# Kernel optimization log

Measured on AMD Instinct MI355X. Metric: run time of the kernel, lower is better.

## Reference

```python
import jax, jax.numpy as jnp
import numpy as np

D_MODEL = 1024
N_HEAD = 16
D_HEAD = D_MODEL // N_HEAD
SEQ = 1024
RLEN = 2 * SEQ
BATCH = 4
LN_EPS = 1e-5


def setup_inputs() -> dict:
    key = jax.random.key(0)
    ks = jax.random.split(key, 12)
    s = 0.02
    return {
        "h": jax.random.normal(ks[0], (SEQ, BATCH, D_MODEL), jnp.float32),
        "r": jax.random.normal(ks[1], (RLEN, BATCH, D_MODEL), jnp.float32),
        "q_w": jax.random.normal(ks[2], (D_MODEL, N_HEAD, D_HEAD), jnp.float32) * s,
        "k_w": jax.random.normal(ks[3], (D_MODEL, N_HEAD, D_HEAD), jnp.float32) * s,
        "v_w": jax.random.normal(ks[4], (D_MODEL, N_HEAD, D_HEAD), jnp.float32) * s,
        "o_w": jax.random.normal(ks[5], (D_MODEL, N_HEAD, D_HEAD), jnp.float32) * s,
        "r_w": jax.random.normal(ks[6], (D_MODEL, N_HEAD, D_HEAD), jnp.float32) * s,
        "r_r_bias": jax.random.normal(ks[7], (N_HEAD, D_HEAD), jnp.float32) * s,
        "r_w_bias": jax.random.normal(ks[8], (N_HEAD, D_HEAD), jnp.float32) * s,
        "ln_gamma": jnp.ones((D_MODEL,), jnp.float32),
        "ln_beta": jnp.zeros((D_MODEL,), jnp.float32),
    }


def rel_shift_bnij(x, klen):
    # x: [b, n, i, j]; Transformer-XL relative-shift trick
    b, n, i, j = x.shape
    x = x.reshape(b, n, j, i)[:, :, 1:, :].reshape(b, n, i, j - 1)
    return x[:, :, :, :klen]


def reference(h, r, q_w, k_w, v_w, o_w, r_w, r_r_bias, r_w_bias, ln_gamma, ln_beta):
    scale = 1.0 / np.sqrt(D_HEAD).astype(np.float32)
    # projections: i=seq, b=batch, n=heads, d=head dim
    q_head = jnp.einsum('ibh,hnd->ibnd', h, q_w)
    k_head = jnp.einsum('ibh,hnd->ibnd', h, k_w)
    v_head = jnp.einsum('ibh,hnd->ibnd', h, v_w)
    k_head_r = jnp.einsum('ibh,hnd->ibnd', r, r_w)
    # content and position attention scores
    ac = jnp.einsum('ibnd,jbnd->bnij', q_head + r_w_bias, k_head)
    bd = jnp.einsum('ibnd,jbnd->bnij', q_head + r_r_bias, k_head_r)
    bd = rel_shift_bnij(bd, klen=ac.shape[3])
    attn_prob = jax.nn.softmax((ac + bd) * scale, axis=3)  # dropout is identity at eval
    attn_vec = jnp.einsum('bnij,jbnd->ibnd', attn_prob, v_head)
    attn_out = jnp.einsum('ibnd,hnd->ibh', attn_vec, o_w) + h  # residual
    mu = jnp.mean(attn_out, axis=-1, keepdims=True)
    var = jnp.var(attn_out, axis=-1, keepdims=True)
    return (attn_out - mu) / jnp.sqrt(var + LN_EPS) * ln_gamma + ln_beta
```

## Files before the change

### kernel.cpp

```cpp
#include <hip/hip_runtime.h>
#include <stdint.h>


typedef __attribute__((ext_vector_type(8))) short v8s;
typedef __attribute__((ext_vector_type(4))) float v4f;

__device__ __forceinline__ uint16_t f2b(float x) {
    uint32_t u = __builtin_bit_cast(uint32_t, x);
    u += 0x7fffu + ((u >> 16) & 1u);
    return (uint16_t)(u >> 16);
}

__device__ __forceinline__ void gld16(const void* g, void* lds) {
    __builtin_amdgcn_global_load_lds(
        (const __attribute__((address_space(1))) uint32_t*)g,
        (__attribute__((address_space(3))) uint32_t*)lds, 16, 0, 0);
}

__global__ __launch_bounds__(256) void convert_cast(
    const float4* __restrict__ h4, const float4* __restrict__ r4,
    const float4* __restrict__ w4,
    uint64_t* __restrict__ hB, uint64_t* __restrict__ rB, uint64_t* __restrict__ owB)
{
    const int total = 1048576 + 2097152 + 262144;
    for (int i = blockIdx.x * 256 + threadIdx.x; i < total; i += gridDim.x * 256) {
        float4 v; uint64_t* dst; int idx;
        if (i < 1048576)      { idx = i;           v = h4[idx]; dst = hB; }
        else if (i < 3145728) { idx = i - 1048576; v = r4[idx]; dst = rB; }
        else                  { idx = i - 3145728; v = w4[idx]; dst = owB; }
        uint64_t p = (uint64_t)f2b(v.x) | ((uint64_t)f2b(v.y) << 16)
                   | ((uint64_t)f2b(v.z) << 32) | ((uint64_t)f2b(v.w) << 48);
        dst[idx] = p;
    }
}

__global__ __launch_bounds__(256) void transpose_w(
    const float* __restrict__ q_w, const float* __restrict__ k_w,
    const float* __restrict__ v_w, const float* __restrict__ r_w,
    uint16_t* __restrict__ Wcat, uint16_t* __restrict__ rwT)
{
    __shared__ float t[64][65];
    const int n0 = blockIdx.x * 64, h0 = blockIdx.y * 64, z = blockIdx.z;
    const float* src = (z == 0) ? q_w : (z == 1) ? k_w : (z == 2) ? v_w : r_w;
    uint16_t* dst = (z == 3) ? rwT : Wcat + (size_t)z * 1048576;
    const int tid = threadIdx.x;
#pragma unroll
    for (int q = 0; q < 16; ++q) {
        int idx = q * 256 + tid, rr = idx >> 6, cc = idx & 63;
        t[rr][cc] = src[(size_t)(h0 + rr) * 1024 + n0 + cc];
    }
    __syncthreads();
#pragma unroll
    for (int q = 0; q < 16; ++q) {
        int idx = q * 256 + tid, rr = idx >> 6, cc = idx & 63;
        dst[(size_t)(n0 + rr) * 1024 + h0 + cc] = f2b(t[cc][rr]);
    }
}

template<int MODE>
__global__ __launch_bounds__(256) void gemm_bt(
    const uint16_t* __restrict__ A, const uint16_t* __restrict__ B, int K,
    uint16_t* __restrict__ o0, uint16_t* __restrict__ o1,
    uint16_t* __restrict__ o2, uint16_t* __restrict__ o3,
    const float* __restrict__ bias0, const float* __restrict__ bias1,
    float* __restrict__ fo, const float* __restrict__ fres)
{
    __shared__ __align__(16) uint16_t As[128 * 64];
    __shared__ __align__(16) uint16_t Bs[128 * 64];
    const int tid = threadIdx.x;
    const int w = tid >> 6, lane = tid & 63;
    const int g = lane >> 4, c15 = lane & 15;
    const int m0 = blockIdx.y * 128, n0 = blockIdx.x * 128;
    const int wr = w >> 1, wc = w & 1;

    int rowq[4], colq[4];
#pragma unroll
    for (int q = 0; q < 4; ++q) {
        int D = (w * 4 + q) * 1024 + lane * 16;
        int row = D >> 7;
        rowq[q] = row;
        colq[q] = (D & 127) ^ ((row & 7) << 4);
    }

    v4f acc[4][4];
#pragma unroll
    for (int i = 0; i < 4; ++i)
#pragma unroll
        for (int j = 0; j < 4; ++j) acc[i][j] = v4f{0.f, 0.f, 0.f, 0.f};

    const char* Abase = (const char*)(A + (size_t)m0 * K);
    const char* Bbase = (const char*)(B + (size_t)n0 * K);
    const size_t ld = (size_t)K * 2;

    for (int kb = 0; kb < K; kb += 64) {
        if (kb) __syncthreads();
#pragma unroll
        for (int q = 0; q < 4; ++q) {
            gld16(Abase + (size_t)rowq[q] * ld + (size_t)kb * 2 + colq[q],
                  (char*)As + (w * 4 + q) * 1024);
            gld16(Bbase + (size_t)rowq[q] * ld + (size_t)kb * 2 + colq[q],
                  (char*)Bs + (w * 4 + q) * 1024);
        }
        asm volatile("s_waitcnt vmcnt(0)" ::: "memory");
        __syncthreads();

        v8s af[4][2], bf[4][2];
#pragma unroll
        for (int mi = 0; mi < 4; ++mi) {
            int row = wr * 64 + mi * 16 + c15;
#pragma unroll
            for (int ks = 0; ks < 2; ++ks) {
                int cl = ks * 64 + g * 16;
                af[mi][ks] = *(const v8s*)((const char*)As + row * 128 + (cl ^ ((row & 7) << 4)));
            }
        }
#pragma unroll
        for (int ni = 0; ni < 4; ++ni) {
            int row = wc * 64 + ni * 16 + c15;
#pragma unroll
            for (int ks = 0; ks < 2; ++ks) {
                int cl = ks * 64 + g * 16;
                bf[ni][ks] = *(const v8s*)((const char*)Bs + row * 128 + (cl ^ ((row & 7) << 4)));
            }
        }
#pragma unroll
        for (int mi = 0; mi < 4; ++mi)
#pragma unroll
            for (int ni = 0; ni < 4; ++ni)
#pragma unroll
                for (int ks = 0; ks < 2; ++ks)
                    acc[mi][ni] = __builtin_amdgcn_mfma_f32_16x16x32_bf16(
                        af[mi][ks], bf[ni][ks], acc[mi][ni], 0, 0, 0);
    }

#pragma unroll
    for (int mi = 0; mi < 4; ++mi)
#pragma unroll
        for (int ni = 0; ni < 4; ++ni)
#pragma unroll
            for (int t = 0; t < 4; ++t) {
                int row = m0 + wr * 64 + mi * 16 + g * 4 + t;
                int col = n0 + wc * 64 + ni * 16 + c15;
                float v = acc[mi][ni][t];
                if (MODE == 0) {
                    int seg = col >> 10, nd = col & 1023;
                    int i = row >> 2, b = row & 3, n = nd >> 6, d = nd & 63;
                    int bn = b * 16 + n;
                    if (seg == 0) {
                        o0[(bn << 16) + (i << 6) + d] = f2b(v + bias0[nd]);
                        o1[(bn << 16) + (i << 6) + d] = f2b(v + bias1[nd]);
                    } else if (seg == 1) {
                        o2[(bn << 16) + (i << 6) + d] = f2b(v);
                    } else {
                        int il = i & 63;
                        int iperm = (i & ~63) | ((il & 15) * 4 + (il >> 4));
                        o3[(bn << 16) + (d << 10) + iperm] = f2b(v);
                    }
                } else if (MODE == 1) {
                    int j = row >> 2, b = row & 3, n = col >> 6, d = col & 63;
                    int bn = b * 16 + n;
                    o0[(bn << 17) + (j << 6) + d] = f2b(v);
                } else {
                    size_t idx = (size_t)row * 1024 + col;
                    fo[idx] = v + fres[idx];
                }
            }
}

__global__ __launch_bounds__(512, 4) void attn_kernel(
    const uint16_t* __restrict__ Qw, const uint16_t* __restrict__ Qr,
    const uint16_t* __restrict__ Kt, const uint16_t* __restrict__ Vt,
    const uint16_t* __restrict__ Kr, uint16_t* __restrict__ AV)
{
    __shared__ __align__(16) uint16_t Ks[2][4096];
    __shared__ __align__(16) uint16_t Vs[2][4096];
    __shared__ __align__(16) uint16_t Krs[16384];
    __shared__ __align__(16) uint16_t Ptl[8][1024];

    const int tid = threadIdx.x, w = tid >> 6, lane = tid & 63;
    const int g = lane >> 4, c15 = lane & 15;
    const int bid = blockIdx.x;
    const int xcd = bid & 7, slot = bid >> 3;
    const int it = slot & 7, bn = ((slot >> 3) << 3) | xcd;
    const int b = bn >> 4, n = bn & 15;
    const int i0 = it * 128, i0w = i0 + w * 16;
    const int B0 = 897 - i0;

    const uint16_t* qwp = Qw + ((size_t)bn << 16);
    const uint16_t* qrp = Qr + ((size_t)bn << 16);
    const char* ktp = (const char*)(Kt + ((size_t)bn << 16));
    const char* vtp = (const char*)(Vt + ((size_t)bn << 16));
    const char* krp = (const char*)(Kr + ((size_t)bn << 17));

    const int rsub = lane >> 3;
    const int csrc = ((lane & 7) ^ rsub) << 4;
    const int dsto = lane * 16;
    const int swz = (c15 & 7) << 4;

    int sl[4], esel[4];
#pragma unroll
    for (int t = 0; t < 4; ++t) {
        int e = 15 + c15 - (g * 4 + t);
        sl[t] = g * 16 + (e & 15);
        esel[t] = e >> 4;
    }

    v8s qwf[2], qrf[2];
#pragma unroll
    for (int ks = 0; ks < 2; ++ks) {
        qwf[ks] = *(const v8s*)(qwp + ((i0w + c15) << 6) + ks * 32 + g * 8);
        qrf[ks] = *(const v8s*)(qrp + ((i0w + c15) << 6) + ks * 32 + g * 8);
    }

    v4f acc_o[4];
    float psac[4];
#pragma unroll
    for (int df = 0; df < 4; ++df) acc_o[df] = v4f{0.f, 0.f, 0.f, 0.f};
#pragma unroll
    for (int t = 0; t < 4; ++t) psac[t] = 0.f;

    uint16_t* Ptw = Ptl[w];
    const float SCL = 0.18033688f;
    const float MB8 = 11.54156032f;

    gld16(ktp + (size_t)(w * 8 + rsub) * 128 + csrc,
          (char*)Ks[0] + w * 1024 + dsto);
    gld16(vtp + (size_t)(w * 8 + rsub) * 2048 + csrc,
          (char*)Vs[0] + w * 1024 + dsto);
#pragma unroll
    for (int qq = 0; qq < 3; ++qq) {
        const int chunk = qq * 8 + w;
        const int rg = B0 + chunk * 8 + rsub;
        gld16(krp + (size_t)rg * 128 + csrc, (char*)Krs + chunk * 1024 + dsto);
    }
    asm volatile("s_waitcnt vmcnt(0)" ::: "memory");
    __syncthreads();

    for (int jt = 0; jt < 16; ++jt) {
        const int cur = jt & 1;
        if (jt < 15) {
            const int j1 = (jt + 1) * 64;
            gld16(ktp + (size_t)(j1 + w * 8 + rsub) * 128 + csrc,
                  (char*)Ks[cur ^ 1] + w * 1024 + dsto);
            gld16(vtp + (size_t)(w * 8 + rsub) * 2048 + j1 * 2 + csrc,
                  (char*)Vs[cur ^ 1] + w * 1024 + dsto);
            const int sbase = (192 + 64 * jt) & 255;
            int rg = B0 + 192 + 64 * jt + w * 8 + rsub;
            rg = rg > 2047 ? 2047 : rg;
            gld16(krp + (size_t)rg * 128 + csrc,
                  (char*)Krs + (sbase + w * 8) * 128 + dsto);
        }

        v4f ac[4];
#pragma unroll
        for (int jf = 0; jf < 4; ++jf) ac[jf] = v4f{0.f, 0.f, 0.f, 0.f};
        v4f pp[5];
#pragma unroll
        for (int pf = 0; pf < 5; ++pf) pp[pf] = v4f{0.f, 0.f, 0.f, 0.f};

        __builtin_amdgcn_s_setprio(1);
#pragma unroll
        for (int jf = 0; jf < 4; ++jf) {
            const char* krow = (const char*)Ks[cur] + (jf * 16 + c15) * 128;
#pragma unroll
            for (int ks = 0; ks < 2; ++ks) {
                v8s kf = *(const v8s*)(krow + ((ks * 64 + g * 16) ^ swz));
                ac[jf] = __builtin_amdgcn_mfma_f32_16x16x32_bf16(qwf[ks], kf, ac[jf], 0, 0, 0);
            }
        }
        const int krbase = 64 * jt + 112 - 16 * w + c15;
#pragma unroll
        for (int pf = 0; pf < 5; ++pf) {
            const int sltr = (krbase + 16 * pf) & 255;
            const char* krow = (const char*)Krs + sltr * 128;
#pragma unroll
            for (int ks = 0; ks < 2; ++ks) {
                v8s krf = *(const v8s*)(krow + ((ks * 64 + g * 16) ^ swz));
                pp[pf] = __builtin_amdgcn_mfma_f32_16x16x32_bf16(qrf[ks], krf, pp[pf], 0, 0, 0);
            }
        }
        __builtin_amdgcn_s_setprio(0);

        float spp[5][4];
#pragma unroll
        for (int pf = 0; pf < 5; ++pf)
#pragma unroll
            for (int t = 0; t < 4; ++t)
                spp[pf][t] = __shfl(pp[pf][t], sl[t]);

#pragma unroll
        for (int t = 0; t < 4; ++t) {
            float p[4];
#pragma unroll
            for (int jf = 0; jf < 4; ++jf) {
                float bd = esel[t] ? spp[jf + 1][t] : spp[jf][t];
                p[jf] = exp2f((ac[jf][t] + bd) * SCL - MB8);
                psac[t] += p[jf];
            }
            uint32_t w0 = (uint32_t)f2b(p[0]) | ((uint32_t)f2b(p[1]) << 16);
            uint32_t w1 = (uint32_t)f2b(p[2]) | ((uint32_t)f2b(p[3]) << 16);
            const int rw = g * 4 + t;
            *(uint2*)((char*)Ptw + rw * 128 + ((c15 * 8) ^ ((rw & 7) << 4))) =
                uint2{w0, w1};
        }
        asm volatile("s_waitcnt lgkmcnt(0)" ::: "memory");

        v8s pa[2];
#pragma unroll
        for (int ks = 0; ks < 2; ++ks)
            pa[ks] = *(const v8s*)((const char*)Ptw + c15 * 128 + ((ks * 64 + g * 16) ^ swz));
        __builtin_amdgcn_s_setprio(1);
#pragma unroll
        for (int df = 0; df < 4; ++df) {
            const char* vrow = (const char*)Vs[cur] + (df * 16 + c15) * 128;
#pragma unroll
            for (int ks = 0; ks < 2; ++ks) {
                v8s vf = *(const v8s*)(vrow + ((ks * 64 + g * 16) ^ swz));
                acc_o[df] = __builtin_amdgcn_mfma_f32_16x16x32_bf16(pa[ks], vf, acc_o[df], 0, 0, 0);
            }
        }
        __builtin_amdgcn_s_setprio(0);

        asm volatile("s_waitcnt vmcnt(0)" ::: "memory");
        __syncthreads();
    }

    float rinv[4];
#pragma unroll
    for (int t = 0; t < 4; ++t) {
        float l = psac[t];
#pragma unroll
        for (int m = 1; m < 16; m <<= 1) l += __shfl_xor(l, m);
        rinv[t] = 1.0f / l;
    }
#pragma unroll
    for (int df = 0; df < 4; ++df)
#pragma unroll
        for (int t = 0; t < 4; ++t) {
            int i = i0w + g * 4 + t;
            int d = df * 16 + c15;
            AV[((size_t)(i * 4 + b) << 10) + n * 64 + d] =
                f2b(acc_o[df][t] * rinv[t]);
        }
}

__global__ __launch_bounds__(256) void ln_kernel(
    const float* __restrict__ AO, const float* __restrict__ gamma,
    const float* __restrict__ beta, float* __restrict__ out)
{
    const int w = threadIdx.x >> 6, lane = threadIdx.x & 63;
    const int row = blockIdx.x * 4 + w;
    const float4* src = (const float4*)(AO + (size_t)row * 1024);
    float4 v[4];
    float s = 0.f, sq = 0.f;
#pragma unroll
    for (int q = 0; q < 4; ++q) {
        v[q] = src[lane + q * 64];
        s += v[q].x + v[q].y + v[q].z + v[q].w;
        sq += v[q].x * v[q].x + v[q].y * v[q].y + v[q].z * v[q].z + v[q].w * v[q].w;
    }
#pragma unroll
    for (int m = 1; m < 64; m <<= 1) { s += __shfl_xor(s, m); sq += __shfl_xor(sq, m); }
    float mean = s * (1.f / 1024.f);
    float var = sq * (1.f / 1024.f) - mean * mean;
    float rstd = rsqrtf(var + 1e-5f);
    const float4* g4 = (const float4*)gamma;
    const float4* b4 = (const float4*)beta;
    float4* o4 = (float4*)(out + (size_t)row * 1024);
#pragma unroll
    for (int q = 0; q < 4; ++q) {
        float4 gg = g4[lane + q * 64], bb = b4[lane + q * 64], vv = v[q], r;
        r.x = (vv.x - mean) * rstd * gg.x + bb.x;
        r.y = (vv.y - mean) * rstd * gg.y + bb.y;
        r.z = (vv.z - mean) * rstd * gg.z + bb.z;
        r.w = (vv.w - mean) * rstd * gg.w + bb.w;
        o4[lane + q * 64] = r;
    }
}

extern "C" void kernel_launch(void* const* d_in, const int* in_sizes, int n_in,
                              void* d_out, int out_size, void* d_ws, size_t ws_size,
                              hipStream_t stream)
{
    const float* h        = (const float*)d_in[0];
    const float* r        = (const float*)d_in[1];
    const float* q_w      = (const float*)d_in[2];
    const float* k_w      = (const float*)d_in[3];
    const float* v_w      = (const float*)d_in[4];
    const float* o_w      = (const float*)d_in[5];
    const float* r_w      = (const float*)d_in[6];
    const float* r_r_bias = (const float*)d_in[7];
    const float* r_w_bias = (const float*)d_in[8];
    const float* ln_gamma = (const float*)d_in[9];
    const float* ln_beta  = (const float*)d_in[10];
    float* out = (float*)d_out;

    char* ws = (char*)d_ws;
    const size_t MB = 1u << 20;
    uint16_t* hB   = (uint16_t*)(ws + 0);
    uint16_t* rB   = (uint16_t*)(ws + 8 * MB);
    uint16_t* Wcat = (uint16_t*)(ws + 24 * MB);
    uint16_t* rwT  = (uint16_t*)(ws + 30 * MB);
    uint16_t* owB  = (uint16_t*)(ws + 32 * MB);
    uint16_t* Qw   = (uint16_t*)(ws + 34 * MB);
    uint16_t* Qr   = (uint16_t*)(ws + 42 * MB);
    uint16_t* Kt   = (uint16_t*)(ws + 50 * MB);
    uint16_t* Vt   = (uint16_t*)(ws + 58 * MB);
    uint16_t* Kr   = (uint16_t*)(ws + 66 * MB);
    uint16_t* AV   = hB;
    float*    AO   = (float*)rB;

    convert_cast<<<2048, 256, 0, stream>>>((const float4*)h, (const float4*)r,
                                           (const float4*)o_w,
                                           (uint64_t*)hB, (uint64_t*)rB, (uint64_t*)owB);
    transpose_w<<<dim3(16, 16, 4), 256, 0, stream>>>(q_w, k_w, v_w, r_w, Wcat, rwT);
    gemm_bt<0><<<dim3(24, 32), 256, 0, stream>>>(hB, Wcat, 1024,
        Qw, Qr, Kt, Vt, r_w_bias, r_r_bias, nullptr, nullptr);
    gemm_bt<1><<<dim3(8, 64), 256, 0, stream>>>(rB, rwT, 1024,
        Kr, nullptr, nullptr, nullptr, nullptr, nullptr, nullptr, nullptr);
    attn_kernel<<<512, 512, 0, stream>>>(Qw, Qr, Kt, Vt, Kr, AV);
    gemm_bt<2><<<dim3(8, 32), 256, 0, stream>>>(AV, owB, 1024,
        nullptr, nullptr, nullptr, nullptr, nullptr, nullptr, AO, h);
    ln_kernel<<<1024, 256, 0, stream>>>(AO, ln_gamma, ln_beta, out);
}
```

Baseline: 187.1 us.

## Merge prep kernels and projection GEMMs into single launches; shrink output GEMM tile

The cast and weight-transpose kernels are merged into one prep launch that picks its branch by block index. The QKV and relative-key projection GEMMs become one launch of 1280 blocks. The output-projection GEMM now uses 64x128 tiles, doubling its grid to 512 blocks so more CUs are busy. This cuts two kernel launches and their tail gaps, at the cost of branchy kernels and less reuse per block in the output GEMM.

```diff
diff --git a/kernel.cpp b/kernel.cpp
--- a/kernel.cpp
+++ b/kernel.cpp
@@ -17,74 +17,85 @@
         (__attribute__((address_space(3))) uint32_t*)lds, 16, 0, 0);
 }
 
-__global__ __launch_bounds__(256) void convert_cast(
-    const float4* __restrict__ h4, const float4* __restrict__ r4,
-    const float4* __restrict__ w4,
-    uint64_t* __restrict__ hB, uint64_t* __restrict__ rB, uint64_t* __restrict__ owB)
-{
-    const int total = 1048576 + 2097152 + 262144;
-    for (int i = blockIdx.x * 256 + threadIdx.x; i < total; i += gridDim.x * 256) {
-        float4 v; uint64_t* dst; int idx;
-        if (i < 1048576)      { idx = i;           v = h4[idx]; dst = hB; }
-        else if (i < 3145728) { idx = i - 1048576; v = r4[idx]; dst = rB; }
-        else                  { idx = i - 3145728; v = w4[idx]; dst = owB; }
-        uint64_t p = (uint64_t)f2b(v.x) | ((uint64_t)f2b(v.y) << 16)
-                   | ((uint64_t)f2b(v.z) << 32) | ((uint64_t)f2b(v.w) << 48);
-        dst[idx] = p;
-    }
-}
-
-__global__ __launch_bounds__(256) void transpose_w(
-    const float* __restrict__ q_w, const float* __restrict__ k_w,
-    const float* __restrict__ v_w, const float* __restrict__ r_w,
-    uint16_t* __restrict__ Wcat, uint16_t* __restrict__ rwT)
+__global__ __launch_bounds__(256) void prep_kernel(
+    const float* __restrict__ h, const float* __restrict__ r,
+    const float* __restrict__ o_w, const float* __restrict__ q_w,
+    const float* __restrict__ k_w, const float* __restrict__ v_w,
+    const float* __restrict__ r_w,
+    uint64_t* __restrict__ hB, uint64_t* __restrict__ rB,
+    uint64_t* __restrict__ owB, uint16_t* __restrict__ Wcat,
+    uint16_t* __restrict__ rwT)
 {
     __shared__ float t[64][65];
-    const int n0 = blockIdx.x * 64, h0 = blockIdx.y * 64, z = blockIdx.z;
-    const float* src = (z == 0) ? q_w : (z == 1) ? k_w : (z == 2) ? v_w : r_w;
-    uint16_t* dst = (z == 3) ? rwT : Wcat + (size_t)z * 1048576;
-    const int tid = threadIdx.x;
-#pragma unroll
-    for (int q = 0; q < 16; ++q) {
-        int idx = q * 256 + tid, rr = idx >> 6, cc = idx & 63;
-        t[rr][cc] = src[(size_t)(h0 + rr) * 1024 + n0 + cc];
-    }
-    __syncthreads();
-#pragma unroll
-    for (int q = 0; q < 16; ++q) {
-        int idx = q * 256 + tid, rr = idx >> 6, cc = idx & 63;
-        dst[(size_t)(n0 + rr) * 1024 + h0 + cc] = f2b(t[cc][rr]);
-    }
-}
-
-template<int MODE>
-__global__ __launch_bounds__(256) void gemm_bt(
+    const int bid = blockIdx.x, tid = threadIdx.x;
+    if (bid < 1024) {
+        const int tx = bid & 15, ty = (bid >> 4) & 15, z = bid >> 8;
+        const int n0 = tx * 64, h0 = ty * 64;
+        const float* src = (z == 0) ? q_w : (z == 1) ? k_w : (z == 2) ? v_w : r_w;
+        uint16_t* dst = (z == 3) ? rwT : Wcat + (size_t)z * 1048576;
+#pragma unroll
+        for (int q = 0; q < 16; ++q) {
+            int idx = q * 256 + tid, rr = idx >> 6, cc = idx & 63;
+            t[rr][cc] = src[(size_t)(h0 + rr) * 1024 + n0 + cc];
+        }
+        __syncthreads();
+#pragma unroll
+        for (int q = 0; q < 16; ++q) {
+            int idx = q * 256 + tid, rr = idx >> 6, cc = idx & 63;
+            dst[(size_t)(n0 + rr) * 1024 + h0 + cc] = f2b(t[cc][rr]);
+        }
+    } else {
+        const float4* h4 = (const float4*)h;
+        const float4* r4 = (const float4*)r;
+        const float4* w4 = (const float4*)o_w;
+        const int total = 1048576 + 2097152 + 262144;
+        for (int i = (bid - 1024) * 256 + tid; i < total; i += 2048 * 256) {
+            float4 v; uint64_t* dst; int idx;
+            if (i < 1048576)      { idx = i;           v = h4[idx]; dst = hB; }
+            else if (i < 3145728) { idx = i - 1048576; v = r4[idx]; dst = rB; }
+            else                  { idx = i - 3145728; v = w4[idx]; dst = owB; }
+            uint64_t p = (uint64_t)f2b(v.x) | ((uint64_t)f2b(v.y) << 16)
+                       | ((uint64_t)f2b(v.z) << 32) | ((uint64_t)f2b(v.w) << 48);
+            dst[idx] = p;
+        }
+    }
+}
+
+template<int MODE, int MI>
+__device__ __forceinline__ void gemm_body(
     const uint16_t* __restrict__ A, const uint16_t* __restrict__ B, int K,
+    int bx, int by, uint16_t* As, uint16_t* Bs,
     uint16_t* __restrict__ o0, uint16_t* __restrict__ o1,
     uint16_t* __restrict__ o2, uint16_t* __restrict__ o3,
     const float* __restrict__ bias0, const float* __restrict__ bias1,
     float* __restrict__ fo, const float* __restrict__ fres)
 {
-    __shared__ __align__(16) uint16_t As[128 * 64];
-    __shared__ __align__(16) uint16_t Bs[128 * 64];
     const int tid = threadIdx.x;
     const int w = tid >> 6, lane = tid & 63;
     const int g = lane >> 4, c15 = lane & 15;
-    const int m0 = blockIdx.y * 128, n0 = blockIdx.x * 128;
+    const int m0 = by * (MI * 32), n0 = bx * 128;
     const int wr = w >> 1, wc = w & 1;
 
-    int rowq[4], colq[4];
+    int rowA[MI], colA[MI];
+#pragma unroll
+    for (int q = 0; q < MI; ++q) {
+        int D = (w * MI + q) * 1024 + lane * 16;
+        int row = D >> 7;
+        rowA[q] = row;
+        colA[q] = (D & 127) ^ ((row & 7) << 4);
+    }
+    int rowB[4], colB[4];
 #pragma unroll
     for (int q = 0; q < 4; ++q) {
         int D = (w * 4 + q) * 1024 + lane * 16;
         int row = D >> 7;
-        rowq[q] = row;
-        colq[q] = (D & 127) ^ ((row & 7) << 4);
-    }
-
-    v4f acc[4][4];
-#pragma unroll
-    for (int i = 0; i < 4; ++i)
+        rowB[q] = row;
+        colB[q] = (D & 127) ^ ((row & 7) << 4);
+    }
+
+    v4f acc[MI][4];
+#pragma unroll
+    for (int i = 0; i < MI; ++i)
 #pragma unroll
         for (int j = 0; j < 4; ++j) acc[i][j] = v4f{0.f, 0.f, 0.f, 0.f};
 
@@ -95,19 +106,20 @@
     for (int kb = 0; kb < K; kb += 64) {
         if (kb) __syncthreads();
 #pragma unroll
-        for (int q = 0; q < 4; ++q) {
-            gld16(Abase + (size_t)rowq[q] * ld + (size_t)kb * 2 + colq[q],
-                  (char*)As + (w * 4 + q) * 1024);
-            gld16(Bbase + (size_t)rowq[q] * ld + (size_t)kb * 2 + colq[q],
+        for (int q = 0; q < MI; ++q)
+            gld16(Abase + (size_t)rowA[q] * ld + (size_t)kb * 2 + colA[q],
+                  (char*)As + (w * MI + q) * 1024);
+#pragma unroll
+        for (int q = 0; q < 4; ++q)
+            gld16(Bbase + (size_t)rowB[q] * ld + (size_t)kb * 2 + colB[q],
                   (char*)Bs + (w * 4 + q) * 1024);
-        }
         asm volatile("s_waitcnt vmcnt(0)" ::: "memory");
         __syncthreads();
 
-        v8s af[4][2], bf[4][2];
-#pragma unroll
-        for (int mi = 0; mi < 4; ++mi) {
-            int row = wr * 64 + mi * 16 + c15;
+        v8s af[MI][2], bf[4][2];
+#pragma unroll
+        for (int mi = 0; mi < MI; ++mi) {
+            int row = wr * (MI * 16) + mi * 16 + c15;
 #pragma unroll
             for (int ks = 0; ks < 2; ++ks) {
                 int cl = ks * 64 + g * 16;
@@ -124,7 +136,7 @@
             }
         }
 #pragma unroll
-        for (int mi = 0; mi < 4; ++mi)
+        for (int mi = 0; mi < MI; ++mi)
 #pragma unroll
             for (int ni = 0; ni < 4; ++ni)
 #pragma unroll
@@ -134,12 +146,12 @@
     }
 
 #pragma unroll
-    for (int mi = 0; mi < 4; ++mi)
+    for (int mi = 0; mi < MI; ++mi)
 #pragma unroll
         for (int ni = 0; ni < 4; ++ni)
 #pragma unroll
             for (int t = 0; t < 4; ++t) {
-                int row = m0 + wr * 64 + mi * 16 + g * 4 + t;
+                int row = m0 + wr * (MI * 16) + mi * 16 + g * 4 + t;
                 int col = n0 + wc * 64 + ni * 16 + c15;
                 float v = acc[mi][ni][t];
                 if (MODE == 0) {
@@ -167,6 +179,39 @@
             }
 }
 
+__global__ __launch_bounds__(256) void gemm_qkvr(
+    const uint16_t* __restrict__ hB, const uint16_t* __restrict__ Wcat,
+    const uint16_t* __restrict__ rB, const uint16_t* __restrict__ rwT,
+    uint16_t* __restrict__ Qw, uint16_t* __restrict__ Qr,
+    uint16_t* __restrict__ Kt, uint16_t* __restrict__ Vt,
+    uint16_t* __restrict__ Kr,
+    const float* __restrict__ b0, const float* __restrict__ b1)
+{
+    __shared__ __align__(16) uint16_t As[128 * 64];
+    __shared__ __align__(16) uint16_t Bs[128 * 64];
+    const int bid = blockIdx.x;
+    if (bid < 768) {
+        gemm_body<0, 4>(hB, Wcat, 1024, bid % 24, bid / 24, As, Bs,
+                        Qw, Qr, Kt, Vt, b0, b1, nullptr, nullptr);
+    } else {
+        const int b2 = bid - 768;
+        gemm_body<1, 4>(rB, rwT, 1024, b2 % 8, b2 / 8, As, Bs,
+                        Kr, nullptr, nullptr, nullptr, nullptr, nullptr,
+                        nullptr, nullptr);
+    }
+}
+
+__global__ __launch_bounds__(256) void gemm_out(
+    const uint16_t* __restrict__ AV, const uint16_t* __restrict__ owB,
+    float* __restrict__ AO, const float* __restrict__ hres)
+{
+    __shared__ __align__(16) uint16_t As[64 * 64];
+    __shared__ __align__(16) uint16_t Bs[128 * 64];
+    gemm_body<2, 2>(AV, owB, 1024, blockIdx.x % 8, blockIdx.x / 8, As, Bs,
+                    nullptr, nullptr, nullptr, nullptr, nullptr, nullptr,
+                    AO, hres);
+}
+
 __global__ __launch_bounds__(512, 4) void attn_kernel(
     const uint16_t* __restrict__ Qw, const uint16_t* __restrict__ Qr,
     const uint16_t* __restrict__ Kt, const uint16_t* __restrict__ Vt,
@@ -410,16 +455,12 @@
     uint16_t* AV   = hB;
     float*    AO   = (float*)rB;
 
-    convert_cast<<<2048, 256, 0, stream>>>((const float4*)h, (const float4*)r,
-                                           (const float4*)o_w,
-                                           (uint64_t*)hB, (uint64_t*)rB, (uint64_t*)owB);
-    transpose_w<<<dim3(16, 16, 4), 256, 0, stream>>>(q_w, k_w, v_w, r_w, Wcat, rwT);
-    gemm_bt<0><<<dim3(24, 32), 256, 0, stream>>>(hB, Wcat, 1024,
-        Qw, Qr, Kt, Vt, r_w_bias, r_r_bias, nullptr, nullptr);
-    gemm_bt<1><<<dim3(8, 64), 256, 0, stream>>>(rB, rwT, 1024,
-        Kr, nullptr, nullptr, nullptr, nullptr, nullptr, nullptr, nullptr);
+    prep_kernel<<<3072, 256, 0, stream>>>(h, r, o_w, q_w, k_w, v_w, r_w,
+                                          (uint64_t*)hB, (uint64_t*)rB,
+                                          (uint64_t*)owB, Wcat, rwT);
+    gemm_qkvr<<<1280, 256, 0, stream>>>(hB, Wcat, rB, rwT,
+                                        Qw, Qr, Kt, Vt, Kr, r_w_bias, r_r_bias);
     attn_kernel<<<512, 512, 0, stream>>>(Qw, Qr, Kt, Vt, Kr, AV);
-    gemm_bt<2><<<dim3(8, 32), 256, 0, stream>>>(AV, owB, 1024,
-        nullptr, nullptr, nullptr, nullptr, nullptr, nullptr, AO, h);
+    gemm_out<<<512, 256, 0, stream>>>(AV, owB, AO, h);
     ln_kernel<<<1024, 256, 0, stream>>>(AO, ln_gamma, ln_beta, out);
 }
```

After: 160.4 us. -14.3%, faster.
